# Kernel optimization log

Measured on AMD Instinct MI355X. Metric: run time of the kernel, lower is better.

The kernel has to match this reference:

```python
import jax, jax.numpy as jnp
import numpy as np

B, T, C, H = 16, 2048, 1024, 64

def setup_inputs() -> dict:
    key = jax.random.key(0)
    kx, kq, kk, kv = jax.random.split(key, 4)
    x = jax.random.normal(kx, (B, T, C), dtype=jnp.float32)
    Wq = jax.random.normal(kq, (C, H), dtype=jnp.float32) * (C ** -0.5)
    Wk = jax.random.normal(kk, (C, H), dtype=jnp.float32) * (C ** -0.5)
    Wv = jax.random.normal(kv, (C, H), dtype=jnp.float32) * (C ** -0.5)
    return {"x": x, "Wq": Wq, "Wk": Wk, "Wv": Wv}

def reference(x, Wq, Wk, Wv):
    # q,k,v: [B,T,H]
    q = jnp.einsum('btc,ch->bth', x, Wq)
    k = jnp.einsum('btc,ch->bth', x, Wk)
    v = jnp.einsum('btc,ch->bth', x, Wv)
    scale = k.shape[-1] ** -0.5
    # scores: [B,T,T], causal mask then softmax (dropout=0 -> identity)
    w = jnp.einsum('bth,bsh->bts', q, k) * scale
    causal = jnp.tril(jnp.ones((x.shape[1], x.shape[1]), dtype=bool))
    w = jnp.where(causal[None, :, :], w, -jnp.inf)
    w = jax.nn.softmax(w, axis=-1)
    out = jnp.einsum('bts,bsh->bth', w, v)
    return out
```

## Files before the change

kernel.cpp:

```cpp
#include <hip/hip_runtime.h>


#define B_ 16
#define T_ 2048
#define C_ 1024
#define H_ 64
#define QK_ELEMS (B_ * T_ * H_)

typedef float  f32x4  __attribute__((ext_vector_type(4)));
typedef __bf16 bf16x8 __attribute__((ext_vector_type(8)));
typedef __bf16 bf16x4 __attribute__((ext_vector_type(4)));

__device__ __forceinline__ void glds16(const void* g, void* l) {
    __builtin_amdgcn_global_load_lds(
        (const __attribute__((address_space(1))) void*)g,
        (__attribute__((address_space(3))) void*)l, 16, 0, 0);
}

__global__ __launch_bounds__(256) void wt_kernel(const float* __restrict__ Wq,
                                                 const float* __restrict__ Wk,
                                                 const float* __restrict__ Wv,
                                                 __bf16* __restrict__ Wt) {
    __shared__ float tl[64][65];
    const int mat = blockIdx.x >> 4;
    const int c0  = (blockIdx.x & 15) * 64;
    const float* W = (mat == 0) ? Wq : (mat == 1) ? Wk : Wv;
    const int t  = threadIdx.x;
    const int r4 = t >> 6;
    const int cc = t & 63;
#pragma unroll
    for (int i = 0; i < 16; i++) {
        const int c = r4 + i * 4;
        tl[c][cc] = W[(size_t)(c0 + c) * H_ + cc];
    }
    __syncthreads();
#pragma unroll
    for (int i = 0; i < 16; i++) {
        const int h = r4 + i * 4;
        const int cc2 = ((((cc >> 3) ^ (h & 7)) << 3) | (cc & 7));
        Wt[(size_t)mat * 65536 + (size_t)h * C_ + c0 + cc2] = (__bf16)tl[cc][h];
    }
}

__global__ __launch_bounds__(256) void qkv_kernel(const float* __restrict__ x,
                                                  const __bf16* __restrict__ Wt,
                                                  __bf16* __restrict__ Qw,
                                                  __bf16* __restrict__ Kw,
                                                  __bf16* __restrict__ Vtw) {
    __shared__ __align__(16) __bf16 Alds[2][64 * 72];
    __shared__ __align__(16) __bf16 Blds[2][192 * 64];

    const int tid  = threadIdx.x;
    const int w    = tid >> 6;
    const int lane = tid & 63;
    const int quad = lane >> 4;
    const int l15  = lane & 15;
    const int wm   = (w & 1) * 32;
    const int wn   = (w >> 1) * 96;
    const int m0   = blockIdx.x * 64;

    f32x4 acc[12];
#pragma unroll
    for (int i = 0; i < 12; i++) acc[i] = (f32x4){0.f, 0.f, 0.f, 0.f};

    const int ar = tid >> 3;
    const int ac = (tid & 7) * 8;
    const float* xA = x + (size_t)(m0 + ar) * C_ + ac;
    const __bf16* bsrc = Wt + (size_t)(w * 48 + (lane >> 3)) * C_ + (lane & 7) * 8;

    float4 a[2][4];
    auto loadA = [&](int slot, int k0) {
        a[slot][0] = *(const float4*)(xA + k0);
        a[slot][1] = *(const float4*)(xA + k0 + 4);
        a[slot][2] = *(const float4*)(xA + k0 + 32 * C_);
        a[slot][3] = *(const float4*)(xA + k0 + 32 * C_ + 4);
    };
    auto storeA = [&](int slot, int buf) {
        bf16x8 v0, v1;
        v0[0]=(__bf16)a[slot][0].x; v0[1]=(__bf16)a[slot][0].y;
        v0[2]=(__bf16)a[slot][0].z; v0[3]=(__bf16)a[slot][0].w;
        v0[4]=(__bf16)a[slot][1].x; v0[5]=(__bf16)a[slot][1].y;
        v0[6]=(__bf16)a[slot][1].z; v0[7]=(__bf16)a[slot][1].w;
        v1[0]=(__bf16)a[slot][2].x; v1[1]=(__bf16)a[slot][2].y;
        v1[2]=(__bf16)a[slot][2].z; v1[3]=(__bf16)a[slot][2].w;
        v1[4]=(__bf16)a[slot][3].x; v1[5]=(__bf16)a[slot][3].y;
        v1[6]=(__bf16)a[slot][3].z; v1[7]=(__bf16)a[slot][3].w;
        *(bf16x8*)&Alds[buf][ar * 72 + ac]        = v0;
        *(bf16x8*)&Alds[buf][(ar + 32) * 72 + ac] = v1;
    };
    auto asyncB = [&](int k0, int buf) {
        __bf16* dst = &Blds[buf][(w * 48) * 64];
        const __bf16* src = bsrc + k0;
#pragma unroll
        for (int i = 0; i < 6; i++)
            glds16(src + (size_t)i * 8 * C_, dst + i * 8 * 64);
    };

    loadA(0, 0); loadA(1, 64);
    asyncB(0, 0);
    storeA(0, 0);

    for (int k = 0; k < 16; k++) {
        __syncthreads();
        const int kn = k + 1;
        if (kn < 16) asyncB(kn * 64, kn & 1);
        if (k + 2 < 16) loadA(k & 1, (k + 2) * 64);
        const int buf = k & 1;
#pragma unroll
        for (int kh = 0; kh < 2; kh++) {
            bf16x8 af0 = *(const bf16x8*)&Alds[buf][(wm + l15) * 72 + kh * 32 + quad * 8];
            bf16x8 af1 = *(const bf16x8*)&Alds[buf][(wm + 16 + l15) * 72 + kh * 32 + quad * 8];
            const int ch8 = ((((kh << 2) + quad) ^ (l15 & 7)) << 3);
#pragma unroll
            for (int nt = 0; nt < 6; nt++) {
                bf16x8 bfr = *(const bf16x8*)&Blds[buf][(wn + nt * 16 + l15) * 64 + ch8];
                acc[nt]     = __builtin_amdgcn_mfma_f32_16x16x32_bf16(af0, bfr, acc[nt], 0, 0, 0);
                acc[6 + nt] = __builtin_amdgcn_mfma_f32_16x16x32_bf16(af1, bfr, acc[6 + nt], 0, 0, 0);
            }
        }
        if (kn < 16) storeA(kn & 1, kn & 1);
    }

#pragma unroll
    for (int mt = 0; mt < 2; mt++) {
        const int row0 = m0 + wm + mt * 16 + quad * 4;
#pragma unroll
        for (int nt = 0; nt < 6; nt++) {
            const int col = wn + nt * 16 + l15;
            const f32x4 acv = acc[mt * 6 + nt];
            if (wn + nt * 16 < 64) {
#pragma unroll
                for (int r = 0; r < 4; r++)
                    Qw[(size_t)(row0 + r) * H_ + col] = (__bf16)acv[r];
            } else if (wn + nt * 16 < 128) {
                const int h = col - 64;
#pragma unroll
                for (int r = 0; r < 4; r++) {
                    const int row = row0 + r;
                    const int hs  = (((h >> 3) ^ (row & 7)) << 3) | (h & 7);
                    Kw[(size_t)row * H_ + hs] = (__bf16)acv[r];
                }
            }
        }
    }
    __bf16* Vt_l = &Alds[0][0];
    if (w >= 2) {
#pragma unroll
        for (int mt = 0; mt < 2; mt++) {
            const int t0 = wm + mt * 16 + quad * 4;
#pragma unroll
            for (int nt = 2; nt < 6; nt++) {
                const int h = (nt - 2) * 16 + l15;
                const f32x4 acv = acc[mt * 6 + nt];
                bf16x4 pv;
                pv[0]=(__bf16)acv[0]; pv[1]=(__bf16)acv[1];
                pv[2]=(__bf16)acv[2]; pv[3]=(__bf16)acv[3];
                *(bf16x4*)&Vt_l[h * 72 + t0] = pv;
            }
        }
    }
    __syncthreads();
    if (w >= 2) {
        const int bb   = m0 >> 11;
        const int tblk = m0 & 2047;
#pragma unroll
        for (int i = 0; i < 4; i++) {
            const int hh = (w - 2) * 32 + i * 8 + (lane >> 3);
            const int cs = (((lane & 7) ^ (lane >> 3)) << 3);
            *(bf16x8*)(Vtw + (((size_t)(bb * H_ + hh)) << 11) + tblk + ((lane & 7) << 3)) =
                *(const bf16x8*)&Vt_l[hh * 72 + cs];
        }
    }
}

#define SCALE_LOG2E 0.18033688011112042f

__global__ __launch_bounds__(256) void attn_kernel(const __bf16* __restrict__ Qw,
                                                   const __bf16* __restrict__ Kw,
                                                   const __bf16* __restrict__ Vtw,
                                                   float* __restrict__ Opart,
                                                   float* __restrict__ Lpart) {
    __shared__ __align__(16) __bf16 Klds[2][64 * 64];
    __shared__ __align__(16) __bf16 Vlds[2][64 * 64];
    __shared__ __align__(16) __bf16 Plds[2][4][16 * 72];

    const int tid  = threadIdx.x;
    const int w    = tid >> 6;
    const int lane = tid & 63;
    const int quad = lane >> 4;
    const int l15  = lane & 15;

    const int b   = blockIdx.x & 15;
    const int cid = blockIdx.x >> 4;
    int i, ci;
    if (cid < 16)      { i = 15 - (cid >> 2); ci = cid & 3; }
    else if (cid < 28) { const int u = cid - 16; i = 11 - u / 3; ci = u % 3; }
    else if (cid < 36) { const int u = cid - 28; i = 7 - (u >> 1); ci = u & 1; }
    else               { i = 3 - (cid - 36); ci = 0; }

    const int jmax = 2 * i + 1;
    const int j0 = ci * 8;
    const int j1 = (j0 + 8 < jmax + 1) ? j0 + 8 : jmax + 1;
    const int nj = j1 - j0;
    const int qA0 = 2 * i * 64;
    const size_t bT = (size_t)b * T_;

    const __bf16* qpA = Qw + (bT + qA0 + w * 16 + l15) * H_ + quad * 8;
    const bf16x8 qfA0 = *(const bf16x8*)qpA;
    const bf16x8 qfA1 = *(const bf16x8*)(qpA + 32);
    const bf16x8 qfB0 = *(const bf16x8*)(qpA + 64 * H_);
    const bf16x8 qfB1 = *(const bf16x8*)(qpA + 64 * H_ + 32);

    float lA = 0.f, lB = 0.f;
    f32x4 accA[4], accB[4];
#pragma unroll
    for (int nt = 0; nt < 4; nt++) {
        accA[nt] = (f32x4){0.f, 0.f, 0.f, 0.f};
        accB[nt] = (f32x4){0.f, 0.f, 0.f, 0.f};
    }

    auto stage = [&](int ts0, int buf) {
        const __bf16* Ks = Kw + (bT + ts0) * H_;
        const __bf16* Vs = Vtw + (((size_t)(b * H_)) << 11) + ts0;
#pragma unroll
        for (int c = 0; c < 2; c++) {
            const int g   = w * 2 + c;
            const int row = g * 8 + (lane >> 3);
            const int cb  = (lane & 7) * 8;
            glds16(Ks + (size_t)row * H_ + cb, &Klds[buf][g * 512]);
            glds16(Vs + ((size_t)row << 11) + cb, &Vlds[buf][g * 512]);
        }
    };

    stage(j0 * 64, 0);

    for (int jj = 0; jj < nj; jj++) {
        const int j = j0 + jj;
        __syncthreads();
        if (jj + 1 < nj) stage((j + 1) * 64, (jj + 1) & 1);
        const int buf = jj & 1;
        const bool doA = (j <= 2 * i);
        const int ts0 = j * 64;
        const int qgA = qA0 + w * 16 + l15;

#pragma unroll
        for (int nt = 0; nt < 4; nt++) {
            const __bf16* kb = &Klds[buf][(nt * 16 + l15) * 64];
            bf16x8 kf0 = *(const bf16x8*)(kb + ((quad ^ (l15 & 7)) << 3));
            bf16x8 kf1 = *(const bf16x8*)(kb + (((4 + quad) ^ (l15 & 7)) << 3));
            const int key0 = ts0 + nt * 16 + quad * 4;

            if (doA) {
                f32x4 z = (f32x4){0.f, 0.f, 0.f, 0.f};
                z = __builtin_amdgcn_mfma_f32_16x16x32_bf16(kf0, qfA0, z, 0, 0, 0);
                z = __builtin_amdgcn_mfma_f32_16x16x32_bf16(kf1, qfA1, z, 0, 0, 0);
                bf16x4 pv;
#pragma unroll
                for (int r = 0; r < 4; r++) {
                    float e = exp2f(__builtin_fmaf(z[r], SCALE_LOG2E, -8.0f));
                    if (j == 2 * i && key0 + r > qgA) e = 0.f;
                    pv[r] = (__bf16)e;
                    lA += e;
                }
                *(bf16x4*)&Plds[0][w][l15 * 72 + nt * 16 + quad * 4] = pv;
            }
            {
                f32x4 z = (f32x4){0.f, 0.f, 0.f, 0.f};
                z = __builtin_amdgcn_mfma_f32_16x16x32_bf16(kf0, qfB0, z, 0, 0, 0);
                z = __builtin_amdgcn_mfma_f32_16x16x32_bf16(kf1, qfB1, z, 0, 0, 0);
                bf16x4 pv;
#pragma unroll
                for (int r = 0; r < 4; r++) {
                    float e = exp2f(__builtin_fmaf(z[r], SCALE_LOG2E, -8.0f));
                    if (j == jmax && key0 + r > qgA + 64) e = 0.f;
                    pv[r] = (__bf16)e;
                    lB += e;
                }
                *(bf16x4*)&Plds[1][w][l15 * 72 + nt * 16 + quad * 4] = pv;
            }
        }
        __asm__ __volatile__("s_waitcnt lgkmcnt(0)" ::: "memory");

        const __bf16* prA = &Plds[0][w][l15 * 72];
        const __bf16* prB = &Plds[1][w][l15 * 72];
        bf16x8 pfA0, pfA1;
        if (doA) {
            pfA0 = *(const bf16x8*)(prA + quad * 8);
            pfA1 = *(const bf16x8*)(prA + 32 + quad * 8);
        }
        bf16x8 pfB0 = *(const bf16x8*)(prB + quad * 8);
        bf16x8 pfB1 = *(const bf16x8*)(prB + 32 + quad * 8);
#pragma unroll
        for (int nt = 0; nt < 4; nt++) {
            const __bf16* vb = &Vlds[buf][(nt * 16 + l15) * 64];
            bf16x8 vf0 = *(const bf16x8*)(vb + ((quad ^ (l15 & 7)) << 3));
            bf16x8 vf1 = *(const bf16x8*)(vb + (((4 + quad) ^ (l15 & 7)) << 3));
            if (doA) {
                accA[nt] = __builtin_amdgcn_mfma_f32_16x16x32_bf16(pfA0, vf0, accA[nt], 0, 0, 0);
                accA[nt] = __builtin_amdgcn_mfma_f32_16x16x32_bf16(pfA1, vf1, accA[nt], 0, 0, 0);
            }
            accB[nt] = __builtin_amdgcn_mfma_f32_16x16x32_bf16(pfB0, vf0, accB[nt], 0, 0, 0);
            accB[nt] = __builtin_amdgcn_mfma_f32_16x16x32_bf16(pfB1, vf1, accB[nt], 0, 0, 0);
        }
    }

    lA += __shfl_xor(lA, 16); lA += __shfl_xor(lA, 32);
    lB += __shfl_xor(lB, 16); lB += __shfl_xor(lB, 32);

    const int qiA = 2 * i;
    const int slotA = ((((b << 5) + qiA) << 2) + ci);
    const int slotB = ((((b << 5) + qiA + 1) << 2) + ci);
    float* OpA = Opart + (size_t)slotA * 4096;
    float* OpB = Opart + (size_t)slotB * 4096;
#pragma unroll
    for (int nt = 0; nt < 4; nt++)
#pragma unroll
        for (int r = 0; r < 4; r++) {
            const int o = (w * 16 + quad * 4 + r) * 64 + nt * 16 + l15;
            OpA[o] = accA[nt][r];
            OpB[o] = accB[nt][r];
        }
    if (quad == 0) {
        Lpart[slotA * 64 + w * 16 + l15] = lA;
        Lpart[slotB * 64 + w * 16 + l15] = lB;
    }
}

__global__ __launch_bounds__(256) void reduce_kernel(const float* __restrict__ Opart,
                                                     const float* __restrict__ Lpart,
                                                     float* __restrict__ out) {
    const int b  = blockIdx.x & 15;
    const int qi = blockIdx.x >> 4;
    const int nc = ((qi & ~1) + 9) >> 3;
    const int tid = threadIdx.x;
    const int q  = tid >> 2;
    const int hc = (tid & 3) * 16;
    const int sbase = ((b << 5) + qi) << 2;

    f32x4 s[4];
#pragma unroll
    for (int i = 0; i < 4; i++) s[i] = (f32x4){0.f, 0.f, 0.f, 0.f};
    float l = 0.f;
    for (int ci = 0; ci < nc; ci++) {
        const float* Op = Opart + (size_t)(sbase + ci) * 4096 + q * 64 + hc;
#pragma unroll
        for (int i = 0; i < 4; i++) s[i] += *(const f32x4*)(Op + i * 4);
        l += Lpart[(sbase + ci) * 64 + q];
    }
    const float inv = 1.f / l;
    float* o = out + ((size_t)b * T_ + qi * 64 + q) * H_ + hc;
#pragma unroll
    for (int i = 0; i < 4; i++) {
        f32x4 r = s[i] * inv;
        *(f32x4*)(o + i * 4) = r;
    }
}

extern "C" void kernel_launch(void* const* d_in, const int* in_sizes, int n_in,
                              void* d_out, int out_size, void* d_ws, size_t ws_size,
                              hipStream_t stream) {
    const float* x  = (const float*)d_in[0];
    const float* Wq = (const float*)d_in[1];
    const float* Wk = (const float*)d_in[2];
    const float* Wv = (const float*)d_in[3];
    float* out = (float*)d_out;

    __bf16* Qw  = (__bf16*)d_ws;
    __bf16* Kw  = Qw + QK_ELEMS;
    __bf16* Vtw = Kw + QK_ELEMS;
    __bf16* Wt  = Vtw + QK_ELEMS;
    float* Opart = (float*)((char*)d_ws + 16777216);
    float* Lpart = Opart + (size_t)2048 * 4096;

    wt_kernel<<<dim3(48), dim3(256), 0, stream>>>(Wq, Wk, Wv, Wt);
    qkv_kernel<<<dim3((B_ * T_) / 64), dim3(256), 0, stream>>>(x, Wt, Qw, Kw, Vtw);
    attn_kernel<<<dim3(640), dim3(256), 0, stream>>>(Qw, Kw, Vtw, Opart, Lpart);
    reduce_kernel<<<dim3(512), dim3(256), 0, stream>>>(Opart, Lpart, out);
}
```

Measured before the change: 242.8 us.

## Load x fragments directly into registers, dropping the shared-memory A staging

In the QKV projection kernel each lane now loads its own MFMA A-fragment rows of x from global memory and converts them to bf16 in registers. This replaces the cooperative load into a double-buffered LDS tile and the LDS reads that followed. The change removes LDS traffic and shared memory use for A, and the V-transpose scratch now reuses the B buffer behind an extra barrier. The cost is that each pair of waves sharing the same rows loads x redundantly, and global loads are less coalesced because each lane reads 32-byte pieces from strided rows. Prefetch depth also drops from two iterations to one.

After: 254.9 us. 5.0% more time.

```diff
diff --git a/kernel.cpp b/kernel.cpp
--- a/kernel.cpp
+++ b/kernel.cpp
@@ -47,7 +47,6 @@
                                                   __bf16* __restrict__ Qw,
                                                   __bf16* __restrict__ Kw,
                                                   __bf16* __restrict__ Vtw) {
-    __shared__ __align__(16) __bf16 Alds[2][64 * 72];
     __shared__ __align__(16) __bf16 Blds[2][192 * 64];
 
     const int tid  = threadIdx.x;
@@ -63,31 +62,21 @@
 #pragma unroll
     for (int i = 0; i < 12; i++) acc[i] = (f32x4){0.f, 0.f, 0.f, 0.f};
 
-    const int ar = tid >> 3;
-    const int ac = (tid & 7) * 8;
-    const float* xA = x + (size_t)(m0 + ar) * C_ + ac;
+    const float* xA0 = x + (size_t)(m0 + wm + l15) * C_ + quad * 8;
+    const float* xA1 = xA0 + 16 * C_;
+
+    float4 a[8];
+    auto loadA = [&](int k0) {
+#pragma unroll
+        for (int kh = 0; kh < 2; kh++) {
+            a[kh * 4 + 0] = *(const float4*)(xA0 + k0 + kh * 32);
+            a[kh * 4 + 1] = *(const float4*)(xA0 + k0 + kh * 32 + 4);
+            a[kh * 4 + 2] = *(const float4*)(xA1 + k0 + kh * 32);
+            a[kh * 4 + 3] = *(const float4*)(xA1 + k0 + kh * 32 + 4);
+        }
+    };
+
     const __bf16* bsrc = Wt + (size_t)(w * 48 + (lane >> 3)) * C_ + (lane & 7) * 8;
-
-    float4 a[2][4];
-    auto loadA = [&](int slot, int k0) {
-        a[slot][0] = *(const float4*)(xA + k0);
-        a[slot][1] = *(const float4*)(xA + k0 + 4);
-        a[slot][2] = *(const float4*)(xA + k0 + 32 * C_);
-        a[slot][3] = *(const float4*)(xA + k0 + 32 * C_ + 4);
-    };
-    auto storeA = [&](int slot, int buf) {
-        bf16x8 v0, v1;
-        v0[0]=(__bf16)a[slot][0].x; v0[1]=(__bf16)a[slot][0].y;
-        v0[2]=(__bf16)a[slot][0].z; v0[3]=(__bf16)a[slot][0].w;
-        v0[4]=(__bf16)a[slot][1].x; v0[5]=(__bf16)a[slot][1].y;
-        v0[6]=(__bf16)a[slot][1].z; v0[7]=(__bf16)a[slot][1].w;
-        v1[0]=(__bf16)a[slot][2].x; v1[1]=(__bf16)a[slot][2].y;
-        v1[2]=(__bf16)a[slot][2].z; v1[3]=(__bf16)a[slot][2].w;
-        v1[4]=(__bf16)a[slot][3].x; v1[5]=(__bf16)a[slot][3].y;
-        v1[6]=(__bf16)a[slot][3].z; v1[7]=(__bf16)a[slot][3].w;
-        *(bf16x8*)&Alds[buf][ar * 72 + ac]        = v0;
-        *(bf16x8*)&Alds[buf][(ar + 32) * 72 + ac] = v1;
-    };
     auto asyncB = [&](int k0, int buf) {
         __bf16* dst = &Blds[buf][(w * 48) * 64];
         const __bf16* src = bsrc + k0;
@@ -96,29 +85,38 @@
             glds16(src + (size_t)i * 8 * C_, dst + i * 8 * 64);
     };
 
-    loadA(0, 0); loadA(1, 64);
     asyncB(0, 0);
-    storeA(0, 0);
+    loadA(0);
 
     for (int k = 0; k < 16; k++) {
         __syncthreads();
+
+        bf16x8 af[2][2];
+#pragma unroll
+        for (int kh = 0; kh < 2; kh++)
+#pragma unroll
+            for (int mt = 0; mt < 2; mt++) {
+                const float4 p = a[kh * 4 + mt * 2 + 0];
+                const float4 q = a[kh * 4 + mt * 2 + 1];
+                bf16x8 v;
+                v[0]=(__bf16)p.x; v[1]=(__bf16)p.y; v[2]=(__bf16)p.z; v[3]=(__bf16)p.w;
+                v[4]=(__bf16)q.x; v[5]=(__bf16)q.y; v[6]=(__bf16)q.z; v[7]=(__bf16)q.w;
+                af[mt][kh] = v;
+            }
+
         const int kn = k + 1;
-        if (kn < 16) asyncB(kn * 64, kn & 1);
-        if (k + 2 < 16) loadA(k & 1, (k + 2) * 64);
+        if (kn < 16) { asyncB(kn * 64, kn & 1); loadA(kn * 64); }
         const int buf = k & 1;
 #pragma unroll
         for (int kh = 0; kh < 2; kh++) {
-            bf16x8 af0 = *(const bf16x8*)&Alds[buf][(wm + l15) * 72 + kh * 32 + quad * 8];
-            bf16x8 af1 = *(const bf16x8*)&Alds[buf][(wm + 16 + l15) * 72 + kh * 32 + quad * 8];
             const int ch8 = ((((kh << 2) + quad) ^ (l15 & 7)) << 3);
 #pragma unroll
             for (int nt = 0; nt < 6; nt++) {
                 bf16x8 bfr = *(const bf16x8*)&Blds[buf][(wn + nt * 16 + l15) * 64 + ch8];
-                acc[nt]     = __builtin_amdgcn_mfma_f32_16x16x32_bf16(af0, bfr, acc[nt], 0, 0, 0);
-                acc[6 + nt] = __builtin_amdgcn_mfma_f32_16x16x32_bf16(af1, bfr, acc[6 + nt], 0, 0, 0);
-            }
-        }
-        if (kn < 16) storeA(kn & 1, kn & 1);
+                acc[nt]     = __builtin_amdgcn_mfma_f32_16x16x32_bf16(af[0][kh], bfr, acc[nt], 0, 0, 0);
+                acc[6 + nt] = __builtin_amdgcn_mfma_f32_16x16x32_bf16(af[1][kh], bfr, acc[6 + nt], 0, 0, 0);
+            }
+        }
     }
 
 #pragma unroll
@@ -143,7 +141,8 @@
             }
         }
     }
-    __bf16* Vt_l = &Alds[0][0];
+    __syncthreads();
+    __bf16* Vt_l = &Blds[0][0];
     if (w >= 2) {
 #pragma unroll
         for (int mt = 0; mt < 2; mt++) {
```
